# Optimization experiments

Hardware: AMD Instinct MI355X
Metric: run time of the kernel (lower is better)

The kernel has to match this reference:

```python
import jax, jax.numpy as jnp
import numpy as np

N, E = 50000, 800000
IN_C, OUT_C, D_EMB = 64, 64, 64
NEG_SLOPE = 0.2  # GDN GraphLayer default leaky_relu slope


def setup_inputs() -> dict:
    key = jax.random.key(0)
    ks = jax.random.split(key, 9)
    return {
        "x": jax.random.normal(ks[0], (N, IN_C), jnp.float32),
        "edge_index": jax.random.randint(ks[1], (2, E), 0, N, dtype=jnp.int32),
        "embedding": jax.random.normal(ks[2], (N, D_EMB), jnp.float32),
        # learned params of GraphLayer (heads=1, concat)
        "W": jax.random.normal(ks[3], (OUT_C, IN_C), jnp.float32) * (1.0 / np.sqrt(IN_C)),
        "att_i": jax.random.normal(ks[4], (OUT_C,), jnp.float32) * 0.1,
        "att_j": jax.random.normal(ks[5], (OUT_C,), jnp.float32) * 0.1,
        "att_em_i": jax.random.normal(ks[6], (D_EMB,), jnp.float32) * 0.1,
        "att_em_j": jax.random.normal(ks[7], (D_EMB,), jnp.float32) * 0.1,
        "bias": jax.random.normal(ks[8], (OUT_C,), jnp.float32) * 0.01,
    }


def reference(x, edge_index, embedding, W, att_i, att_j, att_em_i, att_em_j, bias):
    n = x.shape[0]
    loops = jnp.arange(n, dtype=edge_index.dtype)
    src = jnp.concatenate([edge_index[0], loops])  # message source j
    dst = jnp.concatenate([edge_index[1], loops])  # message target i

    h = x @ W.T  # [N, OUT_C]
    # per-node attention scores (equivalent to cat(h, emb) . cat(att, att_em))
    s_i = h @ att_i + embedding @ att_em_i  # [N]
    s_j = h @ att_j + embedding @ att_em_j  # [N]

    alpha = s_i[dst] + s_j[src]                         # [E+N] edge logits
    alpha = jax.nn.leaky_relu(alpha, NEG_SLOPE)
    # softmax over incoming edges of each destination node
    amax = jax.ops.segment_max(alpha, dst, num_segments=n)
    ex = jnp.exp(alpha - amax[dst])
    denom = jax.ops.segment_sum(ex, dst, num_segments=n)
    alpha = ex / (denom[dst] + 1e-16)

    msg = h[src] * alpha[:, None]                       # [E+N, OUT_C]
    out = jax.ops.segment_sum(msg, dst, num_segments=n) + bias
    return jax.nn.relu(out)
```

## Files before the change

### kernel.cpp

```cpp
#include <hip/hip_runtime.h>
#include <hip/hip_bf16.h>
#include <math.h>

#define NEG_SLOPE 0.2f

#define XTA(k, r) ((k) * 68 + ((r) ^ ((((k) >> 2) & 7) << 2)))

__global__ __launch_bounds__(256) void k_gemm_scatter(
    const float* __restrict__ x, const float* __restrict__ emb,
    const float* __restrict__ W,
    const float* __restrict__ att_i, const float* __restrict__ att_j,
    const float* __restrict__ att_em_i, const float* __restrict__ att_em_j,
    const int* __restrict__ srcA, const int* __restrict__ dstA,
    int* __restrict__ cursor, unsigned short* __restrict__ csr,
    __hip_bfloat16* __restrict__ h, float* __restrict__ s_i,
    float* __restrict__ s_j, int N, int E, int GB, int sh, int nchunks)
{
    __shared__ float lds[8704];
    const int tid = threadIdx.x;

    if ((int)blockIdx.x >= GB) {
        int b     = blockIdx.x - GB;
        int oct   = b & 7;
        int chunk = b >> 3;
        int stride = nchunks * 256;
        for (int e = chunk * 256 + tid; e < E; e += stride) {
            int d = dstA[e];
            if ((d >> sh) == oct) {
                int pos = atomicAdd(&cursor[d], 1);
                if (pos < 64)
                    csr[(size_t)d * 64 + pos] = (unsigned short)srcA[e];
            }
        }
        return;
    }

    float* XT = lds;
    float* WT = lds + 4352;

    const int rbase = blockIdx.x * 64;
    const int valid = min(64, N - rbase);

    #pragma unroll
    for (int i = 0; i < 4; ++i) {
        int idx = i * 256 + tid;
        int r = idx >> 4, m = idx & 15;
        float4 v = make_float4(0.f, 0.f, 0.f, 0.f);
        if (r < valid)
            v = *reinterpret_cast<const float4*>(x + (size_t)(rbase + r) * 64 + 4 * m);
        int k = 4 * m;
        XT[XTA(k + 0, r)] = v.x;
        XT[XTA(k + 1, r)] = v.y;
        XT[XTA(k + 2, r)] = v.z;
        XT[XTA(k + 3, r)] = v.w;
    }
    #pragma unroll
    for (int i = 0; i < 4; ++i) {
        int idx = i * 256 + tid;
        int c = idx >> 4, m = idx & 15;
        float4 v = *reinterpret_cast<const float4*>(W + idx * 4);
        int k = 4 * m;
        WT[(k + 0) * 68 + c] = v.x;
        WT[(k + 1) * 68 + c] = v.y;
        WT[(k + 2) * 68 + c] = v.z;
        WT[(k + 3) * 68 + c] = v.w;
    }
    __syncthreads();

    const int cg = tid & 15, rg = tid >> 4;
    const int c0 = cg * 4, r0 = rg * 4;
    float acc[4][4];
    #pragma unroll
    for (int a = 0; a < 4; ++a)
        #pragma unroll
        for (int b = 0; b < 4; ++b) acc[a][b] = 0.f;

    #pragma unroll 4
    for (int k = 0; k < 64; ++k) {
        float4 wv = *reinterpret_cast<float4*>(&WT[k * 68 + c0]);
        float4 xa = *reinterpret_cast<float4*>(&XT[XTA(k, r0)]);
        float xs[4] = {xa.x, xa.y, xa.z, xa.w};
        float ws[4] = {wv.x, wv.y, wv.z, wv.w};
        #pragma unroll
        for (int a = 0; a < 4; ++a)
            #pragma unroll
            for (int b = 0; b < 4; ++b)
                acc[a][b] = fmaf(ws[a], xs[b], acc[a][b]);
    }

    #pragma unroll
    for (int b = 0; b < 4; ++b) {
        int r = r0 + b;
        if (r < valid) {
            union { __hip_bfloat16 q[4]; uint2 u; } pk;
            pk.q[0] = __float2bfloat16(acc[0][b]);
            pk.q[1] = __float2bfloat16(acc[1][b]);
            pk.q[2] = __float2bfloat16(acc[2][b]);
            pk.q[3] = __float2bfloat16(acc[3][b]);
            *reinterpret_cast<uint2*>(h + (size_t)(rbase + r) * 64 + c0) = pk.u;
        }
    }

    float ai[4], aj[4];
    #pragma unroll
    for (int a = 0; a < 4; ++a) { ai[a] = att_i[c0 + a]; aj[a] = att_j[c0 + a]; }

    __syncthreads();
    float* RED_I = lds;
    float* RED_J = lds + 1088;
    float* EMT   = lds + 4352;

    #pragma unroll
    for (int b = 0; b < 4; ++b) {
        int r = r0 + b;
        float pi = acc[0][b]*ai[0] + acc[1][b]*ai[1] + acc[2][b]*ai[2] + acc[3][b]*ai[3];
        float pj = acc[0][b]*aj[0] + acc[1][b]*aj[1] + acc[2][b]*aj[2] + acc[3][b]*aj[3];
        RED_I[r * 17 + cg] = pi;
        RED_J[r * 17 + cg] = pj;
    }
    #pragma unroll
    for (int i = 0; i < 4; ++i) {
        int idx = i * 256 + tid;
        int r = idx >> 4, m = idx & 15;
        float4 v = make_float4(0.f, 0.f, 0.f, 0.f);
        if (r < valid)
            v = *reinterpret_cast<const float4*>(emb + (size_t)(rbase + r) * 64 + 4 * m);
        int k = 4 * m;
        EMT[(k + 0) * 67 + r] = v.x;
        EMT[(k + 1) * 67 + r] = v.y;
        EMT[(k + 2) * 67 + r] = v.z;
        EMT[(k + 3) * 67 + r] = v.w;
    }
    __syncthreads();

    if (tid < 64 && tid < valid) {
        float ri = 0.f, rj = 0.f;
        #pragma unroll
        for (int j = 0; j < 16; ++j) {
            ri += RED_I[tid * 17 + j];
            rj += RED_J[tid * 17 + j];
        }
        float ei = 0.f, ej = 0.f;
        #pragma unroll 16
        for (int k = 0; k < 64; ++k) {
            float ev = EMT[k * 67 + tid];
            ei = fmaf(ev, att_em_i[k], ei);
            ej = fmaf(ev, att_em_j[k], ej);
        }
        s_i[rbase + tid] = ri + ei;
        s_j[rbase + tid] = rj + ej;
    }
}

__global__ __launch_bounds__(256) void k_aggregate(
    const __hip_bfloat16* __restrict__ h, const float* __restrict__ s_i,
    const float* __restrict__ s_j, const int* __restrict__ cursor,
    const unsigned short* __restrict__ csr, const float* __restrict__ bias,
    float* __restrict__ out, int N)
{
    const int lane = threadIdx.x & 63;
    const int node = (blockIdx.x * blockDim.x + threadIdx.x) >> 6;
    if (node >= N) return;

    int deg_e = cursor[node];
    deg_e = (deg_e > 63) ? 63 : deg_e;
    const int degT = deg_e + 1;
    const float si = s_i[node];

    int s = node;
    if (lane < deg_e) s = csr[(size_t)node * 64 + lane];
    float a = -INFINITY;
    if (lane < degT) {
        a = si + s_j[s];
        a = (a > 0.f) ? a : NEG_SLOPE * a;
    }
    float m = a;
    #pragma unroll
    for (int off = 32; off > 0; off >>= 1) m = fmaxf(m, __shfl_xor(m, off));
    float ex = (lane < degT) ? __expf(a - m) : 0.f;
    float l = ex;
    #pragma unroll
    for (int off = 32; off > 0; off >>= 1) l += __shfl_xor(l, off);

    const int half = lane >> 5;
    const int hc   = lane & 31;
    const unsigned* hp = reinterpret_cast<const unsigned*>(h);
    float ax = 0.f, ay = 0.f;

    int j = 0;
    for (; j + 4 <= degT; j += 4) {
        int j0 = j + half, j1 = j + 2 + half;
        float e0 = __shfl(ex, j0), e1 = __shfl(ex, j1);
        int   t0 = __shfl(s, j0),  t1 = __shfl(s, j1);
        unsigned u0 = hp[(size_t)t0 * 32 + hc];
        unsigned u1 = hp[(size_t)t1 * 32 + hc];
        float lo0 = __uint_as_float(u0 << 16);
        float hi0 = __uint_as_float(u0 & 0xffff0000u);
        float lo1 = __uint_as_float(u1 << 16);
        float hi1 = __uint_as_float(u1 & 0xffff0000u);
        ax = fmaf(e0, lo0, ax); ay = fmaf(e0, hi0, ay);
        ax = fmaf(e1, lo1, ax); ay = fmaf(e1, hi1, ay);
    }
    for (; j < degT; j += 2) {
        int jj = j + half;
        int jc = (jj < degT) ? jj : (degT - 1);
        float e = __shfl(ex, jc);
        int   t = __shfl(s, jc);
        if (jj >= degT) e = 0.f;
        unsigned u = hp[(size_t)t * 32 + hc];
        ax = fmaf(e, __uint_as_float(u << 16), ax);
        ay = fmaf(e, __uint_as_float(u & 0xffff0000u), ay);
    }

    ax += __shfl_xor(ax, 32);
    ay += __shfl_xor(ay, 32);

    if (half == 0) {
        float inv = 1.f / (l + 1e-16f);
        float2 bv = *reinterpret_cast<const float2*>(bias + 2 * hc);
        float2 o;
        o.x = fmaxf(ax * inv + bv.x, 0.f);
        o.y = fmaxf(ay * inv + bv.y, 0.f);
        *reinterpret_cast<float2*>(out + (size_t)node * 64 + 2 * hc) = o;
    }
}

extern "C" void kernel_launch(void* const* d_in, const int* in_sizes, int n_in,
                              void* d_out, int out_size, void* d_ws, size_t ws_size,
                              hipStream_t stream) {
    const float* x        = (const float*)d_in[0];
    const int*   ei       = (const int*)  d_in[1];
    const float* emb      = (const float*)d_in[2];
    const float* W        = (const float*)d_in[3];
    const float* att_i    = (const float*)d_in[4];
    const float* att_j    = (const float*)d_in[5];
    const float* att_em_i = (const float*)d_in[6];
    const float* att_em_j = (const float*)d_in[7];
    const float* bias     = (const float*)d_in[8];
    float* out = (float*)d_out;

    const int N = in_sizes[0] / 64;
    const int E = in_sizes[1] / 2;
    const int* e_src = ei;
    const int* e_dst = ei + E;

    char* ws = (char*)d_ws;
    __hip_bfloat16* h = (__hip_bfloat16*)ws;  ws += (size_t)N * 64 * 2;
    float* s_i     = (float*)ws;  ws += (size_t)N * 4;
    float* s_j     = (float*)ws;  ws += (size_t)N * 4;
    int*   cursor  = (int*)ws;    ws += (size_t)N * 4;
    unsigned short* csr = (unsigned short*)ws;  ws += (size_t)N * 64 * 2;

    int sh = 0;
    while ((1 << sh) < N) ++sh;
    sh -= 3;

    const int GB = (N + 63) / 64;
    const int NCHUNK = 128;

    hipMemsetAsync(cursor, 0, (size_t)N * 4, stream);
    k_gemm_scatter<<<GB + NCHUNK * 8, 256, 0, stream>>>(
        x, emb, W, att_i, att_j, att_em_i, att_em_j,
        e_src, e_dst, cursor, csr, h, s_i, s_j, N, E, GB, sh, NCHUNK);
    k_aggregate<<<(N * 64 + 255) / 256, 256, 0, stream>>>(h, s_i, s_j, cursor,
                                                          csr, bias, out, N);
}
```

Baseline: 164.1 us.

## Fuse memset, GEMM, scatter and aggregate into one cooperative persistent kernel

Replaces the memset plus two kernel launches with a single cooperative kernel of 512 persistent blocks. It zeroes the cursor, runs the GEMM tiles and the CSR scatter, and does the per-node aggregation, separated by grid-wide syncs. It also vectorises the edge reads to int4, unrolls the aggregation gather loop to four loads per iteration, and changes the LDS layout to a swizzled 64-stride form. The aim is to remove launch overhead and inter-kernel gaps. The risks are the cost of grid-wide barriers and the loss of overlap between the GEMM and scatter phases, since each block now runs them one after the other.

```diff
diff --git a/kernel.cpp b/kernel.cpp
--- a/kernel.cpp
+++ b/kernel.cpp
@@ -1,44 +1,27 @@
 #include <hip/hip_runtime.h>
+#include <hip/hip_cooperative_groups.h>
 #include <hip/hip_bf16.h>
 #include <math.h>
 
+namespace cg = cooperative_groups;
+
 #define NEG_SLOPE 0.2f
 
-#define XTA(k, r) ((k) * 68 + ((r) ^ ((((k) >> 2) & 7) << 2)))
-
-__global__ __launch_bounds__(256) void k_gemm_scatter(
+#define XTA(k, r) ((k) * 64 + ((r) ^ ((((k) >> 2) & 7) << 2)))
+
+__device__ __forceinline__ void gemm_tile(
+    float* lds, int t, int tid,
     const float* __restrict__ x, const float* __restrict__ emb,
     const float* __restrict__ W,
     const float* __restrict__ att_i, const float* __restrict__ att_j,
     const float* __restrict__ att_em_i, const float* __restrict__ att_em_j,
-    const int* __restrict__ srcA, const int* __restrict__ dstA,
-    int* __restrict__ cursor, unsigned short* __restrict__ csr,
     __hip_bfloat16* __restrict__ h, float* __restrict__ s_i,
-    float* __restrict__ s_j, int N, int E, int GB, int sh, int nchunks)
-{
-    __shared__ float lds[8704];
-    const int tid = threadIdx.x;
-
-    if ((int)blockIdx.x >= GB) {
-        int b     = blockIdx.x - GB;
-        int oct   = b & 7;
-        int chunk = b >> 3;
-        int stride = nchunks * 256;
-        for (int e = chunk * 256 + tid; e < E; e += stride) {
-            int d = dstA[e];
-            if ((d >> sh) == oct) {
-                int pos = atomicAdd(&cursor[d], 1);
-                if (pos < 64)
-                    csr[(size_t)d * 64 + pos] = (unsigned short)srcA[e];
-            }
-        }
-        return;
-    }
-
+    float* __restrict__ s_j, int N)
+{
     float* XT = lds;
-    float* WT = lds + 4352;
-
-    const int rbase = blockIdx.x * 64;
+    float* WT = lds + 4096;
+
+    const int rbase = t * 64;
     const int valid = min(64, N - rbase);
 
     #pragma unroll
@@ -60,43 +43,43 @@
         int c = idx >> 4, m = idx & 15;
         float4 v = *reinterpret_cast<const float4*>(W + idx * 4);
         int k = 4 * m;
-        WT[(k + 0) * 68 + c] = v.x;
-        WT[(k + 1) * 68 + c] = v.y;
-        WT[(k + 2) * 68 + c] = v.z;
-        WT[(k + 3) * 68 + c] = v.w;
+        WT[XTA(k + 0, c)] = v.x;
+        WT[XTA(k + 1, c)] = v.y;
+        WT[XTA(k + 2, c)] = v.z;
+        WT[XTA(k + 3, c)] = v.w;
     }
     __syncthreads();
 
-    const int cg = tid & 15, rg = tid >> 4;
-    const int c0 = cg * 4, r0 = rg * 4;
+    const int cg_ = tid & 15, rg = tid >> 4;
+    const int c0 = cg_ * 4, r0 = rg * 4;
     float acc[4][4];
     #pragma unroll
     for (int a = 0; a < 4; ++a)
         #pragma unroll
-        for (int b = 0; b < 4; ++b) acc[a][b] = 0.f;
+        for (int q = 0; q < 4; ++q) acc[a][q] = 0.f;
 
     #pragma unroll 4
     for (int k = 0; k < 64; ++k) {
-        float4 wv = *reinterpret_cast<float4*>(&WT[k * 68 + c0]);
+        float4 wv = *reinterpret_cast<float4*>(&WT[XTA(k, c0)]);
         float4 xa = *reinterpret_cast<float4*>(&XT[XTA(k, r0)]);
         float xs[4] = {xa.x, xa.y, xa.z, xa.w};
         float ws[4] = {wv.x, wv.y, wv.z, wv.w};
         #pragma unroll
         for (int a = 0; a < 4; ++a)
             #pragma unroll
-            for (int b = 0; b < 4; ++b)
-                acc[a][b] = fmaf(ws[a], xs[b], acc[a][b]);
-    }
-
-    #pragma unroll
-    for (int b = 0; b < 4; ++b) {
-        int r = r0 + b;
+            for (int q = 0; q < 4; ++q)
+                acc[a][q] = fmaf(ws[a], xs[q], acc[a][q]);
+    }
+
+    #pragma unroll
+    for (int q = 0; q < 4; ++q) {
+        int r = r0 + q;
         if (r < valid) {
-            union { __hip_bfloat16 q[4]; uint2 u; } pk;
-            pk.q[0] = __float2bfloat16(acc[0][b]);
-            pk.q[1] = __float2bfloat16(acc[1][b]);
-            pk.q[2] = __float2bfloat16(acc[2][b]);
-            pk.q[3] = __float2bfloat16(acc[3][b]);
+            union { __hip_bfloat16 p[4]; uint2 u; } pk;
+            pk.p[0] = __float2bfloat16(acc[0][q]);
+            pk.p[1] = __float2bfloat16(acc[1][q]);
+            pk.p[2] = __float2bfloat16(acc[2][q]);
+            pk.p[3] = __float2bfloat16(acc[3][q]);
             *reinterpret_cast<uint2*>(h + (size_t)(rbase + r) * 64 + c0) = pk.u;
         }
     }
@@ -108,15 +91,15 @@
     __syncthreads();
     float* RED_I = lds;
     float* RED_J = lds + 1088;
-    float* EMT   = lds + 4352;
-
-    #pragma unroll
-    for (int b = 0; b < 4; ++b) {
-        int r = r0 + b;
-        float pi = acc[0][b]*ai[0] + acc[1][b]*ai[1] + acc[2][b]*ai[2] + acc[3][b]*ai[3];
-        float pj = acc[0][b]*aj[0] + acc[1][b]*aj[1] + acc[2][b]*aj[2] + acc[3][b]*aj[3];
-        RED_I[r * 17 + cg] = pi;
-        RED_J[r * 17 + cg] = pj;
+    float* EMT   = lds + 4096;
+
+    #pragma unroll
+    for (int q = 0; q < 4; ++q) {
+        int r = r0 + q;
+        float pi = acc[0][q]*ai[0] + acc[1][q]*ai[1] + acc[2][q]*ai[2] + acc[3][q]*ai[3];
+        float pj = acc[0][q]*aj[0] + acc[1][q]*aj[1] + acc[2][q]*aj[2] + acc[3][q]*aj[3];
+        RED_I[r * 17 + cg_] = pi;
+        RED_J[r * 17 + cg_] = pj;
     }
     #pragma unroll
     for (int i = 0; i < 4; ++i) {
@@ -126,10 +109,10 @@
         if (r < valid)
             v = *reinterpret_cast<const float4*>(emb + (size_t)(rbase + r) * 64 + 4 * m);
         int k = 4 * m;
-        EMT[(k + 0) * 67 + r] = v.x;
-        EMT[(k + 1) * 67 + r] = v.y;
-        EMT[(k + 2) * 67 + r] = v.z;
-        EMT[(k + 3) * 67 + r] = v.w;
+        EMT[XTA(k + 0, r)] = v.x;
+        EMT[XTA(k + 1, r)] = v.y;
+        EMT[XTA(k + 2, r)] = v.z;
+        EMT[XTA(k + 3, r)] = v.w;
     }
     __syncthreads();
 
@@ -143,25 +126,54 @@
         float ei = 0.f, ej = 0.f;
         #pragma unroll 16
         for (int k = 0; k < 64; ++k) {
-            float ev = EMT[k * 67 + tid];
+            float ev = EMT[XTA(k, tid)];
             ei = fmaf(ev, att_em_i[k], ei);
             ej = fmaf(ev, att_em_j[k], ej);
         }
         s_i[rbase + tid] = ri + ei;
         s_j[rbase + tid] = rj + ej;
     }
-}
-
-__global__ __launch_bounds__(256) void k_aggregate(
-    const __hip_bfloat16* __restrict__ h, const float* __restrict__ s_i,
-    const float* __restrict__ s_j, const int* __restrict__ cursor,
-    const unsigned short* __restrict__ csr, const float* __restrict__ bias,
-    float* __restrict__ out, int N)
-{
-    const int lane = threadIdx.x & 63;
-    const int node = (blockIdx.x * blockDim.x + threadIdx.x) >> 6;
-    if (node >= N) return;
-
+    __syncthreads();
+}
+
+__device__ __forceinline__ void scatter_part(
+    const int* __restrict__ srcA, const int* __restrict__ dstA,
+    int* __restrict__ cursor, unsigned short* __restrict__ csr,
+    int E, int sh, int oct, int chunk, int npos, int tid)
+{
+    const int E4 = E >> 2;
+    const int4* d4p = reinterpret_cast<const int4*>(dstA);
+    const int4* s4p = reinterpret_cast<const int4*>(srcA);
+    for (int p = chunk * 256 + tid; p < E4; p += npos) {
+        int4 d4 = d4p[p];
+        int4 s4 = s4p[p];
+        int dd[4] = {d4.x, d4.y, d4.z, d4.w};
+        int ss[4] = {s4.x, s4.y, s4.z, s4.w};
+        #pragma unroll
+        for (int i = 0; i < 4; ++i) {
+            if ((dd[i] >> sh) == oct) {
+                int pos = atomicAdd(&cursor[dd[i]], 1);
+                if (pos < 64)
+                    csr[(size_t)dd[i] * 64 + pos] = (unsigned short)ss[i];
+            }
+        }
+    }
+    for (int e = E4 * 4 + chunk * 256 + tid; e < E; e += npos) {
+        int d = dstA[e];
+        if ((d >> sh) == oct) {
+            int pos = atomicAdd(&cursor[d], 1);
+            if (pos < 64)
+                csr[(size_t)d * 64 + pos] = (unsigned short)srcA[e];
+        }
+    }
+}
+
+__device__ __forceinline__ void aggregate_node(
+    int node, int lane, const unsigned* __restrict__ hp,
+    const float* __restrict__ s_i, const float* __restrict__ s_j,
+    const int* __restrict__ cursor, const unsigned short* __restrict__ csr,
+    const float* __restrict__ bias, float* __restrict__ out)
+{
     int deg_e = cursor[node];
     deg_e = (deg_e > 63) ? 63 : deg_e;
     const int degT = deg_e + 1;
@@ -184,22 +196,36 @@
 
     const int half = lane >> 5;
     const int hc   = lane & 31;
-    const unsigned* hp = reinterpret_cast<const unsigned*>(h);
     float ax = 0.f, ay = 0.f;
 
     int j = 0;
-    for (; j + 4 <= degT; j += 4) {
-        int j0 = j + half, j1 = j + 2 + half;
-        float e0 = __shfl(ex, j0), e1 = __shfl(ex, j1);
-        int   t0 = __shfl(s, j0),  t1 = __shfl(s, j1);
+    for (; j + 8 <= degT; j += 8) {
+        float e0 = __shfl(ex, j + half),     e1 = __shfl(ex, j + 2 + half);
+        float e2 = __shfl(ex, j + 4 + half), e3 = __shfl(ex, j + 6 + half);
+        int   t0 = __shfl(s, j + half),      t1 = __shfl(s, j + 2 + half);
+        int   t2 = __shfl(s, j + 4 + half),  t3 = __shfl(s, j + 6 + half);
         unsigned u0 = hp[(size_t)t0 * 32 + hc];
         unsigned u1 = hp[(size_t)t1 * 32 + hc];
-        float lo0 = __uint_as_float(u0 << 16);
-        float hi0 = __uint_as_float(u0 & 0xffff0000u);
-        float lo1 = __uint_as_float(u1 << 16);
-        float hi1 = __uint_as_float(u1 & 0xffff0000u);
-        ax = fmaf(e0, lo0, ax); ay = fmaf(e0, hi0, ay);
-        ax = fmaf(e1, lo1, ax); ay = fmaf(e1, hi1, ay);
+        unsigned u2 = hp[(size_t)t2 * 32 + hc];
+        unsigned u3 = hp[(size_t)t3 * 32 + hc];
+        ax = fmaf(e0, __uint_as_float(u0 << 16), ax);
+        ay = fmaf(e0, __uint_as_float(u0 & 0xffff0000u), ay);
+        ax = fmaf(e1, __uint_as_float(u1 << 16), ax);
+        ay = fmaf(e1, __uint_as_float(u1 & 0xffff0000u), ay);
+        ax = fmaf(e2, __uint_as_float(u2 << 16), ax);
+        ay = fmaf(e2, __uint_as_float(u2 & 0xffff0000u), ay);
+        ax = fmaf(e3, __uint_as_float(u3 << 16), ax);
+        ay = fmaf(e3, __uint_as_float(u3 & 0xffff0000u), ay);
+    }
+    for (; j + 4 <= degT; j += 4) {
+        float e0 = __shfl(ex, j + half), e1 = __shfl(ex, j + 2 + half);
+        int   t0 = __shfl(s, j + half),  t1 = __shfl(s, j + 2 + half);
+        unsigned u0 = hp[(size_t)t0 * 32 + hc];
+        unsigned u1 = hp[(size_t)t1 * 32 + hc];
+        ax = fmaf(e0, __uint_as_float(u0 << 16), ax);
+        ay = fmaf(e0, __uint_as_float(u0 & 0xffff0000u), ay);
+        ax = fmaf(e1, __uint_as_float(u1 << 16), ax);
+        ay = fmaf(e1, __uint_as_float(u1 & 0xffff0000u), ay);
     }
     for (; j < degT; j += 2) {
         int jj = j + half;
@@ -223,6 +249,75 @@
         o.y = fmaxf(ay * inv + bv.y, 0.f);
         *reinterpret_cast<float2*>(out + (size_t)node * 64 + 2 * hc) = o;
     }
+}
+
+__global__ __launch_bounds__(256) void k_mega(
+    const float* __restrict__ x, const float* __restrict__ emb,
+    const float* __restrict__ W,
+    const float* __restrict__ att_i, const float* __restrict__ att_j,
+    const float* __restrict__ att_em_i, const float* __restrict__ att_em_j,
+    const int* __restrict__ srcA, const int* __restrict__ dstA,
+    const float* __restrict__ bias,
+    int* __restrict__ cursor, unsigned short* __restrict__ csr,
+    __hip_bfloat16* __restrict__ h, float* __restrict__ s_i,
+    float* __restrict__ s_j, float* __restrict__ out,
+    int N, int E, int GB, int sh)
+{
+    __shared__ float lds[8192];
+    cg::grid_group grid = cg::this_grid();
+    const int tid = threadIdx.x;
+    const int b   = blockIdx.x;
+    const int NB  = gridDim.x;
+
+    for (int i = b * 256 + tid; i < N; i += NB * 256) cursor[i] = 0;
+    grid.sync();
+
+    for (int t = b; t < GB; t += NB)
+        gemm_tile(lds, t, tid, x, emb, W, att_i, att_j, att_em_i, att_em_j,
+                  h, s_i, s_j, N);
+
+    scatter_part(srcA, dstA, cursor, csr, E, sh, b & 7, b >> 3,
+                 (NB >> 3) * 256, tid);
+    grid.sync();
+
+    const int lane = tid & 63;
+    const unsigned* hp = reinterpret_cast<const unsigned*>(h);
+    for (int node = b * 4 + (tid >> 6); node < N; node += NB * 4)
+        aggregate_node(node, lane, hp, s_i, s_j, cursor, csr, bias, out);
+}
+
+__global__ __launch_bounds__(256) void k_fb_gemm_scatter(
+    const float* __restrict__ x, const float* __restrict__ emb,
+    const float* __restrict__ W,
+    const float* __restrict__ att_i, const float* __restrict__ att_j,
+    const float* __restrict__ att_em_i, const float* __restrict__ att_em_j,
+    const int* __restrict__ srcA, const int* __restrict__ dstA,
+    int* __restrict__ cursor, unsigned short* __restrict__ csr,
+    __hip_bfloat16* __restrict__ h, float* __restrict__ s_i,
+    float* __restrict__ s_j, int N, int E, int GB, int sh, int nchunks)
+{
+    __shared__ float lds[8192];
+    if ((int)blockIdx.x < GB) {
+        gemm_tile(lds, blockIdx.x, threadIdx.x, x, emb, W, att_i, att_j,
+                  att_em_i, att_em_j, h, s_i, s_j, N);
+    } else {
+        int b2 = blockIdx.x - GB;
+        scatter_part(srcA, dstA, cursor, csr, E, sh, b2 & 7, b2 >> 3,
+                     nchunks * 256, threadIdx.x);
+    }
+}
+
+__global__ __launch_bounds__(256) void k_fb_aggregate(
+    const __hip_bfloat16* __restrict__ h, const float* __restrict__ s_i,
+    const float* __restrict__ s_j, const int* __restrict__ cursor,
+    const unsigned short* __restrict__ csr, const float* __restrict__ bias,
+    float* __restrict__ out, int N)
+{
+    const int node = (blockIdx.x * blockDim.x + threadIdx.x) >> 6;
+    if (node >= N) return;
+    aggregate_node(node, threadIdx.x & 63,
+                   reinterpret_cast<const unsigned*>(h),
+                   s_i, s_j, cursor, csr, bias, out);
 }
 
 extern "C" void kernel_launch(void* const* d_in, const int* in_sizes, int n_in,
@@ -255,13 +350,33 @@
     while ((1 << sh) < N) ++sh;
     sh -= 3;
 
-    const int GB = (N + 63) / 64;
-    const int NCHUNK = 128;
-
-    hipMemsetAsync(cursor, 0, (size_t)N * 4, stream);
-    k_gemm_scatter<<<GB + NCHUNK * 8, 256, 0, stream>>>(
-        x, emb, W, att_i, att_j, att_em_i, att_em_j,
-        e_src, e_dst, cursor, csr, h, s_i, s_j, N, E, GB, sh, NCHUNK);
-    k_aggregate<<<(N * 64 + 255) / 256, 256, 0, stream>>>(h, s_i, s_j, cursor,
-                                                          csr, bias, out, N);
-}
+    int GB = (N + 63) / 64;
+    const int NBLK = 512;
+
+    int occ = 0;
+    hipError_t oe = hipOccupancyMaxActiveBlocksPerMultiprocessor(
+        &occ, (const void*)k_mega, 256, 0);
+    bool try_coop = (oe == hipSuccess && occ * 256 >= NBLK);
+
+    hipError_t le = hipErrorUnknown;
+    if (try_coop) {
+        void* args[] = {
+            (void*)&x, (void*)&emb, (void*)&W, (void*)&att_i, (void*)&att_j,
+            (void*)&att_em_i, (void*)&att_em_j, (void*)&e_src, (void*)&e_dst,
+            (void*)&bias, (void*)&cursor, (void*)&csr, (void*)&h,
+            (void*)&s_i, (void*)&s_j, (void*)&out,
+            (void*)&N, (void*)&E, (void*)&GB, (void*)&sh,
+        };
+        le = hipLaunchCooperativeKernel((void*)k_mega, dim3(NBLK), dim3(256),
+                                        args, 0, stream);
+    }
+    if (!try_coop || le != hipSuccess) {
+        const int NCHUNK = 128;
+        hipMemsetAsync(cursor, 0, (size_t)N * 4, stream);
+        k_fb_gemm_scatter<<<GB + NCHUNK * 8, 256, 0, stream>>>(
+            x, emb, W, att_i, att_j, att_em_i, att_em_j,
+            e_src, e_dst, cursor, csr, h, s_i, s_j, N, E, GB, sh, NCHUNK);
+        k_fb_aggregate<<<(N * 64 + 255) / 256, 256, 0, stream>>>(
+            h, s_i, s_j, cursor, csr, bias, out, N);
+    }
+}
```

After: 313.6 us. 1.91x slower.
